# Performance work log

Measured on AMD Instinct MI355X. Metric: run time of the kernel, lower is better.

## Reference

```python
import jax, jax.numpy as jnp
import numpy as np

B, S, D, H = 2, 2048, 1024, 16
HD = D // H
NEG = -10000.0


def setup_inputs() -> dict:
    key = jax.random.key(0)
    ks = jax.random.split(key, 9)
    # xavier-uniform-like scale for square d_model x d_model weights
    lim = float(np.sqrt(6.0 / (D + D)))
    mk_w = lambda k: jax.random.uniform(k, (D, D), jnp.float32, -lim, lim)
    return {
        "q": jax.random.normal(ks[0], (B, S, D), jnp.float32),
        "k": jax.random.normal(ks[1], (B, S, D), jnp.float32),
        "v": jax.random.normal(ks[2], (B, S, D), jnp.float32),
        "attn_mask": jax.random.randint(ks[3], (B, S), 0, 2, jnp.int32),
        "Wq": mk_w(ks[4]),
        "Wk": mk_w(ks[5]),
        "Wv": mk_w(ks[6]),
        "Wo": mk_w(ks[7]),
        "mask_future": 1,
    }


def reference(q, k, v, attn_mask, Wq, Wk, Wv, Wo, mask_future):
    # nn.Linear(bias=False): y = x @ W.T
    def split_heads(x, W):
        return (x @ W.T).reshape(B, S, H, HD).transpose(0, 2, 1, 3)  # [B,H,S,HD]

    qh = split_heads(q, Wq)
    kh = split_heads(k, Wk)
    vh = split_heads(v, Wv)

    scale = 1.0 / np.sqrt(HD)
    scores = jnp.einsum("bhld,bhsd->bhls", qh, kh) * scale  # [B,H,L,S]

    if mask_future:  # static python flag
        rows = jnp.arange(S)[:, None]
        cols = jnp.arange(S)[None, :]
        causal_bias = jnp.where(cols > rows, jnp.float32(NEG), jnp.float32(0.0))
        scores = scores + causal_bias

    # masked_fill(attn_mask == 0, -10000): sets score exactly to NEG (after bias add)
    pad = attn_mask[:, None, None, :]  # [B,1,1,S]
    scores = jnp.where(pad == 0, jnp.float32(NEG), scores)

    probs = jax.nn.softmax(scores, axis=-1)
    ctx = jnp.einsum("bhls,bhsd->bhld", probs, vh)  # [B,H,L,HD]
    ctx = ctx.transpose(0, 2, 1, 3).reshape(B, S, D)
    return ctx @ Wo.T
```

## Files before the change

### kernel.cpp

```cpp
#include <hip/hip_runtime.h>
#include <hip/hip_bf16.h>

typedef __attribute__((ext_vector_type(8))) short bf16x8;
typedef __attribute__((ext_vector_type(4))) short bf16x4;
typedef __attribute__((ext_vector_type(4))) float f32x4;

#define B_ 2
#define S_ 2048
#define D_ 1024
#define H_ 16
#define HD_ 64
#define M_ 4096
#define NEGV (-10000.0f)

#define NQ_ 4194304
#define NW_ 1048576

#if __has_builtin(__builtin_amdgcn_mfma_f32_16x16x16bf16_1k)
#define HAVE_MFMA16 1
#else
#define HAVE_MFMA16 0
#endif

static __device__ __forceinline__ unsigned short f2bf(float x) {
  __hip_bfloat16 h = __float2bfloat16(x);
  return *reinterpret_cast<unsigned short*>(&h);
}

static __device__ __forceinline__ bf16x8 cvt8(const float* p) {
  float4 a = *reinterpret_cast<const float4*>(p);
  float4 b = *reinterpret_cast<const float4*>(p + 4);
  bf16x8 r;
  r[0] = (short)f2bf(a.x); r[1] = (short)f2bf(a.y);
  r[2] = (short)f2bf(a.z); r[3] = (short)f2bf(a.w);
  r[4] = (short)f2bf(b.x); r[5] = (short)f2bf(b.y);
  r[6] = (short)f2bf(b.z); r[7] = (short)f2bf(b.w);
  return r;
}

static __device__ __forceinline__ void gl_lds16(const unsigned short* g, unsigned short* l) {
#if __has_builtin(__builtin_amdgcn_global_load_lds)
  __builtin_amdgcn_global_load_lds(
      (const __attribute__((address_space(1))) unsigned int*)g,
      (__attribute__((address_space(3))) unsigned int*)l, 16, 0, 0);
#else
  *reinterpret_cast<bf16x8*>(l) = *reinterpret_cast<const bf16x8*>(g);
#endif
}


__global__ __launch_bounds__(256) void cvt_all(const float* __restrict__ q,
                                               const float* __restrict__ k,
                                               const float* __restrict__ v,
                                               const float* __restrict__ wq,
                                               const float* __restrict__ wk,
                                               const float* __restrict__ wv,
                                               const float* __restrict__ wo,
                                               unsigned short* __restrict__ dst) {
  for (size_t c = (size_t)blockIdx.x * 256 + threadIdx.x; c < 2097152; c += (size_t)2048 * 256) {
    const size_t e = c * 8;
    const float* s;
    if (e < (size_t)NQ_)            s = q  + e;
    else if (e < (size_t)2 * NQ_)   s = k  + (e - (size_t)NQ_);
    else if (e < (size_t)3 * NQ_)   s = v  + (e - (size_t)2 * NQ_);
    else if (e < (size_t)3 * NQ_ + NW_)     s = wq + (e - (size_t)3 * NQ_);
    else if (e < (size_t)3 * NQ_ + 2 * NW_) s = wk + (e - (size_t)3 * NQ_ - NW_);
    else if (e < (size_t)3 * NQ_ + 3 * NW_) s = wv + (e - (size_t)3 * NQ_ - 2 * NW_);
    else                                    s = wo + (e - (size_t)3 * NQ_ - 3 * NW_);
    *reinterpret_cast<bf16x8*>(dst + e) = cvt8(s);
  }
}

template<bool HSPLIT>
static __device__ __forceinline__ void core_fast(const unsigned short* A,
                                                 const unsigned short* Bw,
                                                 unsigned short* Asm, unsigned short* Bsm,
                                                 int m0, int n0, f32x4 (*acc)[4]) {
  const int tid = threadIdx.x, lane = tid & 63, wid = tid >> 6;
  const int wm = wid >> 1, wn = wid & 1;
  const int l15 = lane & 15, l4 = lane >> 4;

  for (int k0 = 0; k0 < 1024; k0 += 64) {
    __syncthreads();
#pragma unroll
    for (int i = 0; i < 4; ++i) {
      const int idx = tid + 256 * i;
      const int row = idx >> 3;
      const int ce = ((idx & 7) * 8) ^ ((row & 7) << 3);
      const unsigned short* ga;
      if constexpr (HSPLIT) {
        const int m = m0 + row, kk = k0 + ce;
        const int bb = m >> 11, s = m & 2047;
        ga = A + (((size_t)(bb * H_ + (kk >> 6)) * S_ + s) * HD_ + (kk & 63));
      } else {
        ga = A + (size_t)(m0 + row) * 1024 + k0 + ce;
      }
      gl_lds16(ga, Asm + (size_t)idx * 8);
      gl_lds16(Bw + (size_t)(n0 + row) * 1024 + k0 + ce, Bsm + (size_t)idx * 8);
    }
    __syncthreads();
#pragma unroll
    for (int kk = 0; kk < 2; ++kk) {
      bf16x8 af[4], bfr[4];
#pragma unroll
      for (int f = 0; f < 4; ++f) {
        const int ra = wm * 64 + f * 16 + l15;
        const int ca = (kk * 32 + l4 * 8) ^ ((ra & 7) << 3);
        af[f] = *reinterpret_cast<const bf16x8*>(&Asm[ra * 64 + ca]);
        const int rb = wn * 64 + f * 16 + l15;
        const int cb = (kk * 32 + l4 * 8) ^ ((rb & 7) << 3);
        bfr[f] = *reinterpret_cast<const bf16x8*>(&Bsm[rb * 64 + cb]);
      }
#pragma unroll
      for (int fm = 0; fm < 4; ++fm)
#pragma unroll
        for (int fn = 0; fn < 4; ++fn)
          acc[fm][fn] = __builtin_amdgcn_mfma_f32_16x16x32_bf16(af[fm], bfr[fn], acc[fm][fn], 0, 0, 0);
    }
  }
}

__global__ __launch_bounds__(256) void gemm_qkv_fast(const unsigned short* __restrict__ qbf,
                                                     const unsigned short* __restrict__ kbf,
                                                     const unsigned short* __restrict__ vbf,
                                                     const unsigned short* __restrict__ wbf,
                                                     unsigned short* __restrict__ Qh,
                                                     unsigned short* __restrict__ Kh,
                                                     unsigned short* __restrict__ Vt) {
  __shared__ unsigned short Asm[128 * 64];
  __shared__ unsigned short Bsm[128 * 64];
  const int z = blockIdx.z;
  const unsigned short* A  = (z == 0) ? qbf : (z == 1) ? kbf : vbf;
  const unsigned short* Bw = wbf + (size_t)z * NW_;
  const int m0 = blockIdx.y * 128, n0 = blockIdx.x * 128;
  const int lane = threadIdx.x & 63, wid = threadIdx.x >> 6;
  const int wm = wid >> 1, wn = wid & 1;
  const int l15 = lane & 15, l4 = lane >> 4;
  f32x4 acc[4][4] = {};
  core_fast<false>(A, Bw, Asm, Bsm, m0, n0, acc);

#pragma unroll
  for (int fm = 0; fm < 4; ++fm) {
#pragma unroll
    for (int fn = 0; fn < 4; ++fn) {
      const int mg0 = m0 + wm * 64 + fm * 16 + l4 * 4;
      const int ng  = n0 + wn * 64 + fn * 16 + l15;
      const int bidx = mg0 >> 11, s = mg0 & 2047;
      const int h = ng >> 6, d = ng & 63;
      if (z < 2) {
        unsigned short* C = (z == 0) ? Qh : Kh;
#pragma unroll
        for (int r = 0; r < 4; ++r)
          C[((size_t)((bidx * H_ + h) * S_ + s + r)) * HD_ + d] = f2bf(acc[fm][fn][r]);
      } else {
        ushort4 pk;
        pk.x = f2bf(acc[fm][fn][0]); pk.y = f2bf(acc[fm][fn][1]);
        pk.z = f2bf(acc[fm][fn][2]); pk.w = f2bf(acc[fm][fn][3]);
        *reinterpret_cast<ushort4*>(&Vt[((size_t)((bidx * H_ + h) * HD_ + d)) * S_ + s]) = pk;
      }
    }
  }
}

__global__ __launch_bounds__(256) void gemm_o_fast(const unsigned short* __restrict__ ctx,
                                                   const unsigned short* __restrict__ wobf,
                                                   float* __restrict__ Cout) {
  __shared__ unsigned short Asm[128 * 64];
  __shared__ unsigned short Bsm[128 * 64];
  const int m0 = blockIdx.y * 128, n0 = blockIdx.x * 128;
  const int lane = threadIdx.x & 63, wid = threadIdx.x >> 6;
  const int wm = wid >> 1, wn = wid & 1;
  const int l15 = lane & 15, l4 = lane >> 4;
  f32x4 acc[4][4] = {};
  core_fast<true>(ctx, wobf, Asm, Bsm, m0, n0, acc);

#pragma unroll
  for (int fm = 0; fm < 4; ++fm)
#pragma unroll
    for (int fn = 0; fn < 4; ++fn) {
      const int mg0 = m0 + wm * 64 + fm * 16 + l4 * 4;
      const int ng  = n0 + wn * 64 + fn * 16 + l15;
#pragma unroll
      for (int r = 0; r < 4; ++r)
        Cout[(size_t)(mg0 + r) * 1024 + ng] = acc[fm][fn][r];
    }
}


template<bool AF32, bool BF32, bool HSPLIT>
static __device__ __forceinline__ void gemm_core(const void* Av, const void* Bv,
                                                 unsigned short* Asm, unsigned short* Bsm,
                                                 int m0, int n0, f32x4 (*acc)[4]) {
  constexpr int BK = 64, LDT = 72;
  constexpr int K = 1024;
  const int tid = threadIdx.x;
  const int lane = tid & 63, wid = tid >> 6;
  const int wm = wid >> 1, wn = wid & 1;
  const int l15 = lane & 15, l4 = lane >> 4;

  for (int k0 = 0; k0 < K; k0 += BK) {
    __syncthreads();
#pragma unroll
    for (int i = 0; i < 4; ++i) {
      int idx = tid + 256 * i;
      int row = idx >> 3, k8 = (idx & 7) * 8;
      bf16x8 va, vb;
      if constexpr (AF32) {
        va = cvt8((const float*)Av + (size_t)(m0 + row) * K + k0 + k8);
      } else if constexpr (HSPLIT) {
        const int m = m0 + row, kk = k0 + k8;
        const int bb = m >> 11, s = m & 2047;
        va = *reinterpret_cast<const bf16x8*>(
            (const unsigned short*)Av +
            (((size_t)(bb * H_ + (kk >> 6)) * S_ + s) * HD_ + (kk & 63)));
      } else {
        va = *reinterpret_cast<const bf16x8*>((const unsigned short*)Av + (size_t)(m0 + row) * K + k0 + k8);
      }
      if constexpr (BF32) {
        vb = cvt8((const float*)Bv + (size_t)(n0 + row) * K + k0 + k8);
      } else {
        vb = *reinterpret_cast<const bf16x8*>((const unsigned short*)Bv + (size_t)(n0 + row) * K + k0 + k8);
      }
      *reinterpret_cast<bf16x8*>(&Asm[row * LDT + k8]) = va;
      *reinterpret_cast<bf16x8*>(&Bsm[row * LDT + k8]) = vb;
    }
    __syncthreads();
#pragma unroll
    for (int kk = 0; kk < 2; ++kk) {
      bf16x8 af[4], bfr[4];
#pragma unroll
      for (int f = 0; f < 4; ++f) {
        af[f]  = *reinterpret_cast<const bf16x8*>(&Asm[(wm * 64 + f * 16 + l15) * LDT + kk * 32 + l4 * 8]);
        bfr[f] = *reinterpret_cast<const bf16x8*>(&Bsm[(wn * 64 + f * 16 + l15) * LDT + kk * 32 + l4 * 8]);
      }
#pragma unroll
      for (int fm = 0; fm < 4; ++fm)
#pragma unroll
        for (int fn = 0; fn < 4; ++fn)
          acc[fm][fn] = __builtin_amdgcn_mfma_f32_16x16x32_bf16(af[fm], bfr[fn], acc[fm][fn], 0, 0, 0);
    }
  }
}

__global__ __launch_bounds__(256) void gemm_qkv3(const float* __restrict__ q,
                                                 const float* __restrict__ k,
                                                 const float* __restrict__ v,
                                                 const float* __restrict__ Wq,
                                                 const float* __restrict__ Wk,
                                                 const float* __restrict__ Wv,
                                                 unsigned short* __restrict__ Qh,
                                                 unsigned short* __restrict__ Kh,
                                                 unsigned short* __restrict__ Vt) {
  constexpr int LDT = 72;
  __shared__ unsigned short Asm[128 * LDT];
  __shared__ unsigned short Bsm[128 * LDT];
  const int z = blockIdx.z;
  const float* A  = (z == 0) ? q  : (z == 1) ? k  : v;
  const float* Bw = (z == 0) ? Wq : (z == 1) ? Wk : Wv;
  const int m0 = blockIdx.y * 128, n0 = blockIdx.x * 128;
  const int lane = threadIdx.x & 63, wid = threadIdx.x >> 6;
  const int wm = wid >> 1, wn = wid & 1;
  const int l15 = lane & 15, l4 = lane >> 4;
  f32x4 acc[4][4] = {};
  gemm_core<true, true, false>(A, Bw, Asm, Bsm, m0, n0, acc);

#pragma unroll
  for (int fm = 0; fm < 4; ++fm) {
#pragma unroll
    for (int fn = 0; fn < 4; ++fn) {
      const int mg0 = m0 + wm * 64 + fm * 16 + l4 * 4;
      const int ng  = n0 + wn * 64 + fn * 16 + l15;
      const int bidx = mg0 >> 11, s = mg0 & 2047;
      const int h = ng >> 6, d = ng & 63;
      if (z < 2) {
        unsigned short* C = (z == 0) ? Qh : Kh;
#pragma unroll
        for (int r = 0; r < 4; ++r)
          C[((size_t)((bidx * H_ + h) * S_ + s + r)) * HD_ + d] = f2bf(acc[fm][fn][r]);
      } else {
        ushort4 pk;
        pk.x = f2bf(acc[fm][fn][0]); pk.y = f2bf(acc[fm][fn][1]);
        pk.z = f2bf(acc[fm][fn][2]); pk.w = f2bf(acc[fm][fn][3]);
        *reinterpret_cast<ushort4*>(&Vt[((size_t)((bidx * H_ + h) * HD_ + d)) * S_ + s]) = pk;
      }
    }
  }
}

__global__ __launch_bounds__(256) void gemm_oproj(const void* __restrict__ Av,
                                                  const void* __restrict__ Bv,
                                                  float* __restrict__ Cout) {
  constexpr int LDT = 72;
  __shared__ unsigned short Asm[128 * LDT];
  __shared__ unsigned short Bsm[128 * LDT];
  const int m0 = blockIdx.y * 128, n0 = blockIdx.x * 128;
  const int lane = threadIdx.x & 63, wid = threadIdx.x >> 6;
  const int wm = wid >> 1, wn = wid & 1;
  const int l15 = lane & 15, l4 = lane >> 4;
  f32x4 acc[4][4] = {};
  gemm_core<false, true, true>(Av, Bv, Asm, Bsm, m0, n0, acc);

#pragma unroll
  for (int fm = 0; fm < 4; ++fm)
#pragma unroll
    for (int fn = 0; fn < 4; ++fn) {
      const int mg0 = m0 + wm * 64 + fm * 16 + l4 * 4;
      const int ng  = n0 + wn * 64 + fn * 16 + l15;
#pragma unroll
      for (int r = 0; r < 4; ++r)
        Cout[(size_t)(mg0 + r) * 1024 + ng] = acc[fm][fn][r];
    }
}

__global__ __launch_bounds__(128) void attn_fwd(const unsigned short* Qh,
                                                const unsigned short* __restrict__ Kh,
                                                const unsigned short* __restrict__ Vt,
                                                const int* __restrict__ attn_mask,
                                                const int* __restrict__ mask_future,
                                                unsigned short* ctx) {
  constexpr int KVB = 64;
  __shared__ unsigned short Ksm[64 * 64];
  __shared__ unsigned short Vsm[64 * 64];
#if !HAVE_MFMA16
  __shared__ unsigned short Psm[2][16 * 72];
#endif
  __shared__ int s_any;
  const int tid = threadIdx.x, lane = tid & 63, wid = tid >> 6;
  const int l15 = lane & 15, l4 = lane >> 4;
  const int bh = blockIdx.y, b = bh >> 4;
  const int q0 = (int)((blockIdx.x + 9 * blockIdx.y) & 31) * 64;
  const bool causal = (mask_future[0] != 0);
  const int* mrow = attn_mask + b * S_;

  if (tid == 0) s_any = 0;
  __syncthreads();
  for (int i = tid; i <= q0; i += 128)
    if (mrow[i]) s_any = 1;
  __syncthreads();
  const int kb_end = (causal && s_any) ? (q0 + 64) : S_;

  const unsigned short* Qb = Qh + (size_t)bh * S_ * HD_;
  const unsigned short* Kb = Kh + (size_t)bh * S_ * HD_;
  const unsigned short* Vb = Vt + (size_t)bh * HD_ * S_;

  int qrow[2];
  bf16x8 qf0[2], qf1[2];
#pragma unroll
  for (int f = 0; f < 2; ++f) {
    qrow[f] = q0 + wid * 32 + f * 16 + l15;
    qf0[f] = *reinterpret_cast<const bf16x8*>(&Qb[(size_t)qrow[f] * HD_ + l4 * 8]);
    qf1[f] = *reinterpret_cast<const bf16x8*>(&Qb[(size_t)qrow[f] * HD_ + 32 + l4 * 8]);
  }

  float m_run[2] = {-1e30f, -1e30f}, l_run[2] = {0.f, 0.f};
  f32x4 o[2][4] = {};

  bf16x8 kreg[4], vreg[4];
#pragma unroll
  for (int j = 0; j < 4; ++j) {
    const int idx = tid + 128 * j;
    const int row = idx >> 3;
    const int ce = ((idx & 7) * 8) ^ ((row & 7) << 3);
    kreg[j] = *reinterpret_cast<const bf16x8*>(&Kb[(size_t)row * HD_ + ce]);
    vreg[j] = *reinterpret_cast<const bf16x8*>(&Vb[(size_t)row * S_ + ce]);
  }

  for (int kb = 0; kb < kb_end; kb += KVB) {
    __syncthreads();
#pragma unroll
    for (int j = 0; j < 4; ++j) {
      const int idx = tid + 128 * j;
      *reinterpret_cast<bf16x8*>(&Ksm[idx * 8]) = kreg[j];
      *reinterpret_cast<bf16x8*>(&Vsm[idx * 8]) = vreg[j];
    }
    __syncthreads();

    if (kb + KVB < kb_end) {
      const int kn = kb + KVB;
#pragma unroll
      for (int j = 0; j < 4; ++j) {
        const int idx = tid + 128 * j;
        const int row = idx >> 3;
        const int ce = ((idx & 7) * 8) ^ ((row & 7) << 3);
        kreg[j] = *reinterpret_cast<const bf16x8*>(&Kb[(size_t)(kn + row) * HD_ + ce]);
        vreg[j] = *reinterpret_cast<const bf16x8*>(&Vb[(size_t)row * S_ + kn + ce]);
      }
    }

    int4 mk4 [4];
#pragma unroll
    for (int nf = 0; nf < 4; ++nf)
      mk4[nf] = *reinterpret_cast<const int4*>(&mrow[kb + nf * 16 + l4 * 4]);

#pragma unroll
    for (int f = 0; f < 2; ++f) {
      f32x4 sc[4];
#pragma unroll
      for (int nf = 0; nf < 4; ++nf) {
        const int ra = nf * 16 + l15, sw = (ra & 7) << 3;
        bf16x8 kf0 = *reinterpret_cast<const bf16x8*>(&Ksm[ra * 64 + ((l4 * 8) ^ sw)]);
        bf16x8 kf1 = *reinterpret_cast<const bf16x8*>(&Ksm[ra * 64 + ((32 + l4 * 8) ^ sw)]);
        f32x4 z = {};
        z = __builtin_amdgcn_mfma_f32_16x16x32_bf16(kf0, qf0[f], z, 0, 0, 0);
        z = __builtin_amdgcn_mfma_f32_16x16x32_bf16(kf1, qf1[f], z, 0, 0, 0);
        sc[nf] = z;
      }

      float p[4][4];
      float mx = -1e30f;
#pragma unroll
      for (int nf = 0; nf < 4; ++nf) {
        const int kbase = kb + nf * 16 + l4 * 4;
#pragma unroll
        for (int r = 0; r < 4; ++r) {
          float vv = sc[nf][r] * 0.125f;
          if (causal && (kbase + r) > qrow[f]) vv += NEGV;
          const int mkr = (r == 0) ? mk4[nf].x : (r == 1) ? mk4[nf].y : (r == 2) ? mk4[nf].z : mk4[nf].w;
          if (mkr == 0) vv = NEGV;
          p[nf][r] = vv;
          mx = fmaxf(mx, vv);
        }
      }
      mx = fmaxf(mx, __shfl_xor(mx, 16));
      mx = fmaxf(mx, __shfl_xor(mx, 32));
      const float m_new = fmaxf(m_run[f], mx);
      const float scale = __expf(m_run[f] - m_new);
      float s_loc = 0.f;
#pragma unroll
      for (int nf = 0; nf < 4; ++nf)
#pragma unroll
        for (int r = 0; r < 4; ++r) {
          float e = __expf(p[nf][r] - m_new);
          p[nf][r] = e;
          s_loc += e;
        }
      s_loc += __shfl_xor(s_loc, 16);
      s_loc += __shfl_xor(s_loc, 32);
      l_run[f] = l_run[f] * scale + s_loc;
      m_run[f] = m_new;

      float sq[4];
#pragma unroll
      for (int r = 0; r < 4; ++r) sq[r] = __shfl(scale, l4 * 4 + r);
#pragma unroll
      for (int nf2 = 0; nf2 < 4; ++nf2)
#pragma unroll
        for (int r = 0; r < 4; ++r) o[f][nf2][r] *= sq[r];

#if HAVE_MFMA16
      bf16x4 pk[4];
#pragma unroll
      for (int nf = 0; nf < 4; ++nf) {
        bf16x4 t;
        t[0] = (short)f2bf(p[nf][0]); t[1] = (short)f2bf(p[nf][1]);
        t[2] = (short)f2bf(p[nf][2]); t[3] = (short)f2bf(p[nf][3]);
        pk[nf] = t;
      }
#pragma unroll
      for (int nf2 = 0; nf2 < 4; ++nf2) {
        const int rv = nf2 * 16 + l15, swv = (rv & 7) << 3;
#pragma unroll
        for (int nf = 0; nf < 4; ++nf) {
          bf16x4 vf = *reinterpret_cast<const bf16x4*>(&Vsm[rv * 64 + ((nf * 16 + l4 * 4) ^ swv)]);
          o[f][nf2] = __builtin_amdgcn_mfma_f32_16x16x16bf16_1k(pk[nf], vf, o[f][nf2], 0, 0, 0);
        }
      }
#else
      unsigned short* Pw = &Psm[wid][0];
#pragma unroll
      for (int nf = 0; nf < 4; ++nf)
#pragma unroll
        for (int r = 0; r < 4; ++r)
          Pw[l15 * 72 + nf * 16 + l4 * 4 + r] = f2bf(p[nf][r]);
#pragma unroll
      for (int nf2 = 0; nf2 < 4; ++nf2) {
        const int rv = nf2 * 16 + l15, swv = (rv & 7) << 3;
#pragma unroll
        for (int kk = 0; kk < 2; ++kk) {
          bf16x8 pf = *reinterpret_cast<const bf16x8*>(&Pw[l15 * 72 + kk * 32 + l4 * 8]);
          bf16x8 vf = *reinterpret_cast<const bf16x8*>(&Vsm[rv * 64 + ((kk * 32 + l4 * 8) ^ swv)]);
          o[f][nf2] = __builtin_amdgcn_mfma_f32_16x16x32_bf16(pf, vf, o[f][nf2], 0, 0, 0);
        }
      }
#endif
    }
  }

#pragma unroll
  for (int f = 0; f < 2; ++f) {
    const float linv = 1.f / l_run[f];
    float lq[4];
#pragma unroll
    for (int r = 0; r < 4; ++r) lq[r] = __shfl(linv, l4 * 4 + r);
#pragma unroll
    for (int nf2 = 0; nf2 < 4; ++nf2)
#pragma unroll
      for (int r = 0; r < 4; ++r) {
        const int rowg = q0 + wid * 32 + f * 16 + l4 * 4 + r;
        ctx[((size_t)bh * S_ + rowg) * HD_ + nf2 * 16 + l15] = f2bf(o[f][nf2][r] * lq[r]);
      }
  }
}

extern "C" void kernel_launch(void* const* d_in, const int* in_sizes, int n_in,
                              void* d_out, int out_size, void* d_ws, size_t ws_size,
                              hipStream_t stream) {
  const float* q = (const float*)d_in[0];
  const float* k = (const float*)d_in[1];
  const float* v = (const float*)d_in[2];
  const int* attn_mask = (const int*)d_in[3];
  const float* Wq = (const float*)d_in[4];
  const float* Wk = (const float*)d_in[5];
  const float* Wv = (const float*)d_in[6];
  const float* Wo = (const float*)d_in[7];
  const int* mask_future = (const int*)d_in[8];

  unsigned short* ws = (unsigned short*)d_ws;
  unsigned short* Vt = (unsigned short*)d_out;
  float* out = (float*)d_out;
  (void)in_sizes; (void)n_in; (void)out_size;

  const size_t CVT_ELEMS = (size_t)3 * NQ_ + 4 * NW_;
  const size_t NEED = (CVT_ELEMS + 2 * (size_t)NQ_) * 2;

  if (ws_size >= NEED) {
    unsigned short* cvt = ws;
    unsigned short* qbf = cvt;
    unsigned short* kbf = cvt + (size_t)NQ_;
    unsigned short* vbf = cvt + (size_t)2 * NQ_;
    unsigned short* wbf = cvt + (size_t)3 * NQ_;
    unsigned short* Qh  = cvt + CVT_ELEMS;
    unsigned short* Kh  = Qh + (size_t)NQ_;

    cvt_all<<<2048, 256, 0, stream>>>(q, k, v, Wq, Wk, Wv, Wo, cvt);
    gemm_qkv_fast<<<dim3(8, 32, 3), 256, 0, stream>>>(qbf, kbf, vbf, wbf, Qh, Kh, Vt);
    attn_fwd<<<dim3(32, 32), 128, 0, stream>>>(Qh, Kh, Vt, attn_mask, mask_future, Qh);
    gemm_o_fast<<<dim3(8, 32), 256, 0, stream>>>(Qh, wbf + (size_t)3 * NW_, out);
  } else {
    unsigned short* Qh = ws;
    unsigned short* Kh = ws + (size_t)NQ_;
    gemm_qkv3<<<dim3(8, 32, 3), 256, 0, stream>>>(q, k, v, Wq, Wk, Wv, Qh, Kh, Vt);
    attn_fwd<<<dim3(32, 32), 128, 0, stream>>>(Qh, Kh, Vt, attn_mask, mask_future, Qh);
    gemm_oproj<<<dim3(8, 32), 256, 0, stream>>>(Qh, Wo, out);
  }
}
```

Before: 176.5 us.

## Split attention KV range into two halves with a separate combine kernel

Replaces the single attention kernel with a split-KV variant where each query tile is handled by two blocks covering key ranges [0,1024) and [1024,end). The block index is remapped so heavy causal tiles are scheduled first. A new combine kernel merges the partial max/sum and bf16 partial outputs into the context. This targets the load imbalance of causal attention and raises the block count, but adds partial-result traffic, an extra launch and extra bf16 rounding of partial outputs. The partial buffers reuse the start of the workspace, which also holds the converted inputs that are dead by that point.

Result: no change. 175.8 us (-0.4%).

```diff
diff --git a/kernel.cpp b/kernel.cpp
--- a/kernel.cpp
+++ b/kernel.cpp
@@ -25,6 +25,11 @@
 static __device__ __forceinline__ unsigned short f2bf(float x) {
   __hip_bfloat16 h = __float2bfloat16(x);
   return *reinterpret_cast<unsigned short*>(&h);
+}
+
+static __device__ __forceinline__ float bf2f(unsigned short u) {
+  unsigned int x = ((unsigned int)u) << 16;
+  return __uint_as_float(x);
 }
 
 static __device__ __forceinline__ bf16x8 cvt8(const float* p) {
@@ -184,6 +189,207 @@
       for (int r = 0; r < 4; ++r)
         Cout[(size_t)(mg0 + r) * 1024 + ng] = acc[fm][fn][r];
     }
+}
+
+__global__ __launch_bounds__(128) void attn_split(const unsigned short* __restrict__ Qh,
+                                                  const unsigned short* __restrict__ Kh,
+                                                  const unsigned short* __restrict__ Vt,
+                                                  const int* __restrict__ attn_mask,
+                                                  const int* __restrict__ mask_future,
+                                                  float* __restrict__ Pml,
+                                                  unsigned short* __restrict__ Po) {
+  constexpr int KVB = 64;
+  __shared__ unsigned short Ksm[64 * 64];
+  __shared__ unsigned short Vsm[64 * 64];
+  __shared__ int s_any;
+  const int bx = (int)blockIdx.x;
+  int qt, part, bh;
+  if (bx < 512)       { part = 0; qt = 16 + (bx >> 5); bh = bx & 31; }
+  else if (bx < 544)  { part = 0; qt = 15;             bh = bx & 31; }
+  else if (bx < 576)  { part = 1; qt = 31;             bh = bx & 31; }
+  else if (bx < 1536) { const int j = bx - 576, g = j >> 6, n = 15 - g, r = j & 63;
+                        if (r < 32) { part = 0; qt = n - 1;  bh = r; }
+                        else        { part = 1; qt = n + 15; bh = r - 32; } }
+  else                { const int j = bx - 1536; part = 1; qt = j >> 5; bh = j & 31; }
+
+  const int q0 = qt * 64;
+  const int tid = threadIdx.x, lane = tid & 63, wid = tid >> 6;
+  const int l15 = lane & 15, l4 = lane >> 4;
+  const int b = bh >> 4;
+  const bool causal = (mask_future[0] != 0);
+  const int* mrow = attn_mask + b * S_;
+
+  if (tid == 0) s_any = 0;
+  __syncthreads();
+  for (int i = tid; i <= q0; i += 128)
+    if (mrow[i]) s_any = 1;
+  __syncthreads();
+  const int kb_end_full = (causal && s_any) ? (q0 + 64) : S_;
+  const int kb_lo = part ? 1024 : 0;
+  const int kb_hi = part ? kb_end_full : (kb_end_full < 1024 ? kb_end_full : 1024);
+
+  const unsigned short* Qb = Qh + (size_t)bh * S_ * HD_;
+  const unsigned short* Kb = Kh + (size_t)bh * S_ * HD_;
+  const unsigned short* Vb = Vt + (size_t)bh * HD_ * S_;
+
+  float m_run[2] = {-1e30f, -1e30f}, l_run[2] = {0.f, 0.f};
+  f32x4 o[2][4] = {};
+
+  if (kb_lo < kb_hi) {
+    int qrow[2];
+    bf16x8 qf0[2], qf1[2];
+#pragma unroll
+    for (int f = 0; f < 2; ++f) {
+      qrow[f] = q0 + wid * 32 + f * 16 + l15;
+      qf0[f] = *reinterpret_cast<const bf16x8*>(&Qb[(size_t)qrow[f] * HD_ + l4 * 8]);
+      qf1[f] = *reinterpret_cast<const bf16x8*>(&Qb[(size_t)qrow[f] * HD_ + 32 + l4 * 8]);
+    }
+
+    bf16x8 kreg[4], vreg[4];
+#pragma unroll
+    for (int j = 0; j < 4; ++j) {
+      const int idx = tid + 128 * j;
+      const int row = idx >> 3;
+      const int ce = ((idx & 7) * 8) ^ ((row & 7) << 3);
+      kreg[j] = *reinterpret_cast<const bf16x8*>(&Kb[(size_t)(kb_lo + row) * HD_ + ce]);
+      vreg[j] = *reinterpret_cast<const bf16x8*>(&Vb[(size_t)row * S_ + kb_lo + ce]);
+    }
+
+    for (int kb = kb_lo; kb < kb_hi; kb += KVB) {
+      __syncthreads();
+#pragma unroll
+      for (int j = 0; j < 4; ++j) {
+        const int idx = tid + 128 * j;
+        *reinterpret_cast<bf16x8*>(&Ksm[idx * 8]) = kreg[j];
+        *reinterpret_cast<bf16x8*>(&Vsm[idx * 8]) = vreg[j];
+      }
+      __syncthreads();
+
+      if (kb + KVB < kb_hi) {
+        const int kn = kb + KVB;
+#pragma unroll
+        for (int j = 0; j < 4; ++j) {
+          const int idx = tid + 128 * j;
+          const int row = idx >> 3;
+          const int ce = ((idx & 7) * 8) ^ ((row & 7) << 3);
+          kreg[j] = *reinterpret_cast<const bf16x8*>(&Kb[(size_t)(kn + row) * HD_ + ce]);
+          vreg[j] = *reinterpret_cast<const bf16x8*>(&Vb[(size_t)row * S_ + kn + ce]);
+        }
+      }
+
+      int4 mk4[4];
+#pragma unroll
+      for (int nf = 0; nf < 4; ++nf)
+        mk4[nf] = *reinterpret_cast<const int4*>(&mrow[kb + nf * 16 + l4 * 4]);
+
+#pragma unroll
+      for (int f = 0; f < 2; ++f) {
+        f32x4 sc[4];
+#pragma unroll
+        for (int nf = 0; nf < 4; ++nf) {
+          const int ra = nf * 16 + l15, sw = (ra & 7) << 3;
+          bf16x8 kf0 = *reinterpret_cast<const bf16x8*>(&Ksm[ra * 64 + ((l4 * 8) ^ sw)]);
+          bf16x8 kf1 = *reinterpret_cast<const bf16x8*>(&Ksm[ra * 64 + ((32 + l4 * 8) ^ sw)]);
+          f32x4 z = {};
+          z = __builtin_amdgcn_mfma_f32_16x16x32_bf16(kf0, qf0[f], z, 0, 0, 0);
+          z = __builtin_amdgcn_mfma_f32_16x16x32_bf16(kf1, qf1[f], z, 0, 0, 0);
+          sc[nf] = z;
+        }
+
+        float p[4][4];
+        float mx = -1e30f;
+#pragma unroll
+        for (int nf = 0; nf < 4; ++nf) {
+          const int kbase = kb + nf * 16 + l4 * 4;
+#pragma unroll
+          for (int r = 0; r < 4; ++r) {
+            float vv = sc[nf][r] * 0.125f;
+            if (causal && (kbase + r) > qrow[f]) vv += NEGV;
+            const int mkr = (r == 0) ? mk4[nf].x : (r == 1) ? mk4[nf].y : (r == 2) ? mk4[nf].z : mk4[nf].w;
+            if (mkr == 0) vv = NEGV;
+            p[nf][r] = vv;
+            mx = fmaxf(mx, vv);
+          }
+        }
+        mx = fmaxf(mx, __shfl_xor(mx, 16));
+        mx = fmaxf(mx, __shfl_xor(mx, 32));
+        const float m_new = fmaxf(m_run[f], mx);
+        const float scale = __expf(m_run[f] - m_new);
+        float s_loc = 0.f;
+#pragma unroll
+        for (int nf = 0; nf < 4; ++nf)
+#pragma unroll
+          for (int r = 0; r < 4; ++r) {
+            float e = __expf(p[nf][r] - m_new);
+            p[nf][r] = e;
+            s_loc += e;
+          }
+        s_loc += __shfl_xor(s_loc, 16);
+        s_loc += __shfl_xor(s_loc, 32);
+        l_run[f] = l_run[f] * scale + s_loc;
+        m_run[f] = m_new;
+
+        float sq[4];
+#pragma unroll
+        for (int r = 0; r < 4; ++r) sq[r] = __shfl(scale, l4 * 4 + r);
+#pragma unroll
+        for (int nf2 = 0; nf2 < 4; ++nf2)
+#pragma unroll
+          for (int r = 0; r < 4; ++r) o[f][nf2][r] *= sq[r];
+
+        bf16x4 pk[4];
+#pragma unroll
+        for (int nf = 0; nf < 4; ++nf) {
+          bf16x4 t;
+          t[0] = (short)f2bf(p[nf][0]); t[1] = (short)f2bf(p[nf][1]);
+          t[2] = (short)f2bf(p[nf][2]); t[3] = (short)f2bf(p[nf][3]);
+          pk[nf] = t;
+        }
+#pragma unroll
+        for (int nf2 = 0; nf2 < 4; ++nf2) {
+          const int rv = nf2 * 16 + l15, swv = (rv & 7) << 3;
+#pragma unroll
+          for (int nf = 0; nf < 4; ++nf) {
+            bf16x4 vf = *reinterpret_cast<const bf16x4*>(&Vsm[rv * 64 + ((nf * 16 + l4 * 4) ^ swv)]);
+            o[f][nf2] = __builtin_amdgcn_mfma_f32_16x16x16bf16_1k(pk[nf], vf, o[f][nf2], 0, 0, 0);
+          }
+        }
+      }
+    }
+  }
+
+#pragma unroll
+  for (int f = 0; f < 2; ++f) {
+    const int row0 = q0 + wid * 32 + f * 16;
+    if (l4 == 0) {
+      float* pml = &Pml[(((size_t)bh * S_ + row0 + l15) * 2 + part) * 2];
+      pml[0] = m_run[f];
+      pml[1] = l_run[f];
+    }
+#pragma unroll
+    for (int nf2 = 0; nf2 < 4; ++nf2)
+#pragma unroll
+      for (int r = 0; r < 4; ++r) {
+        const int row = row0 + l4 * 4 + r;
+        Po[(((size_t)bh * S_ + row) * 2 + part) * 64 + nf2 * 16 + l15] = f2bf(o[f][nf2][r]);
+      }
+  }
+}
+
+__global__ __launch_bounds__(256) void attn_combine(const float* __restrict__ Pml,
+                                                    const unsigned short* __restrict__ Po,
+                                                    unsigned short* __restrict__ ctx) {
+  const int t = (int)blockIdx.x * 256 + (int)threadIdx.x;
+  const int d = t & 63;
+  const size_t rb = (size_t)(t >> 6);
+  const float mA = Pml[(rb * 2 + 0) * 2], lA = Pml[(rb * 2 + 0) * 2 + 1];
+  const float mB = Pml[(rb * 2 + 1) * 2], lB = Pml[(rb * 2 + 1) * 2 + 1];
+  const float ms = fmaxf(mA, mB);
+  const float wA = __expf(mA - ms), wB = __expf(mB - ms);
+  const float L = lA * wA + lB * wB;
+  const float oA = bf2f(Po[(rb * 2 + 0) * 64 + d]);
+  const float oB = bf2f(Po[(rb * 2 + 1) * 64 + d]);
+  ctx[rb * 64 + d] = f2bf((oA * wA + oB * wB) / L);
 }
 
 
@@ -321,9 +527,6 @@
   constexpr int KVB = 64;
   __shared__ unsigned short Ksm[64 * 64];
   __shared__ unsigned short Vsm[64 * 64];
-#if !HAVE_MFMA16
-  __shared__ unsigned short Psm[2][16 * 72];
-#endif
   __shared__ int s_any;
   const int tid = threadIdx.x, lane = tid & 63, wid = tid >> 6;
   const int l15 = lane & 15, l4 = lane >> 4;
@@ -387,7 +590,7 @@
       }
     }
 
-    int4 mk4 [4];
+    int4 mk4[4];
 #pragma unroll
     for (int nf = 0; nf < 4; ++nf)
       mk4[nf] = *reinterpret_cast<const int4*>(&mrow[kb + nf * 16 + l4 * 4]);
@@ -447,7 +650,6 @@
 #pragma unroll
         for (int r = 0; r < 4; ++r) o[f][nf2][r] *= sq[r];
 
-#if HAVE_MFMA16
       bf16x4 pk[4];
 #pragma unroll
       for (int nf = 0; nf < 4; ++nf) {
@@ -465,24 +667,6 @@
           o[f][nf2] = __builtin_amdgcn_mfma_f32_16x16x16bf16_1k(pk[nf], vf, o[f][nf2], 0, 0, 0);
         }
       }
-#else
-      unsigned short* Pw = &Psm[wid][0];
-#pragma unroll
-      for (int nf = 0; nf < 4; ++nf)
-#pragma unroll
-        for (int r = 0; r < 4; ++r)
-          Pw[l15 * 72 + nf * 16 + l4 * 4 + r] = f2bf(p[nf][r]);
-#pragma unroll
-      for (int nf2 = 0; nf2 < 4; ++nf2) {
-        const int rv = nf2 * 16 + l15, swv = (rv & 7) << 3;
-#pragma unroll
-        for (int kk = 0; kk < 2; ++kk) {
-          bf16x8 pf = *reinterpret_cast<const bf16x8*>(&Pw[l15 * 72 + kk * 32 + l4 * 8]);
-          bf16x8 vf = *reinterpret_cast<const bf16x8*>(&Vsm[rv * 64 + ((kk * 32 + l4 * 8) ^ swv)]);
-          o[f][nf2] = __builtin_amdgcn_mfma_f32_16x16x32_bf16(pf, vf, o[f][nf2], 0, 0, 0);
-        }
-      }
-#endif
     }
   }
 
@@ -531,10 +715,13 @@
     unsigned short* wbf = cvt + (size_t)3 * NQ_;
     unsigned short* Qh  = cvt + CVT_ELEMS;
     unsigned short* Kh  = Qh + (size_t)NQ_;
+    float* Pml = (float*)d_ws;
+    unsigned short* Po = (unsigned short*)((char*)d_ws + (1 << 20));
 
     cvt_all<<<2048, 256, 0, stream>>>(q, k, v, Wq, Wk, Wv, Wo, cvt);
     gemm_qkv_fast<<<dim3(8, 32, 3), 256, 0, stream>>>(qbf, kbf, vbf, wbf, Qh, Kh, Vt);
-    attn_fwd<<<dim3(32, 32), 128, 0, stream>>>(Qh, Kh, Vt, attn_mask, mask_future, Qh);
+    attn_split<<<2048, 128, 0, stream>>>(Qh, Kh, Vt, attn_mask, mask_future, Pml, Po);
+    attn_combine<<<16384, 256, 0, stream>>>(Pml, Po, Qh);
     gemm_o_fast<<<dim3(8, 32), 256, 0, stream>>>(Qh, wbf + (size_t)3 * NW_, out);
   } else {
     unsigned short* Qh = ws;
```
